# Performance work log

Hardware: AMD Instinct MI355X
Metric: run time of the kernel (lower is better)

The kernel has to match this reference:

```python
import jax, jax.numpy as jnp
import numpy as np

BS, T, NOBJ = 16, 32, 100
GLOVE, GEMB, ADIM, GCN_DIM, H, ASPACE, RES = 300, 64, 10, 512, 512, 6, 512


def setup_inputs() -> dict:
    key = jax.random.key(0)
    ks = jax.random.split(key, 34)
    rn = lambda k, shp, s=0.02: (jax.random.normal(k, shp, jnp.float32) * s)
    inp = {}
    inp["target"] = jax.random.normal(ks[0], (BS, T, GLOVE), jnp.float32)
    inp["input_"] = jax.random.normal(ks[1], (BS, T, RES, 1, 1), jnp.float32)
    inp["action_probs"] = jax.random.uniform(ks[2], (BS, T, ASPACE), jnp.float32)
    # symmetric normalized adjacency (D^-1/2 A D^-1/2), as normalize_adj produces
    A_raw = (jax.random.uniform(ks[3], (NOBJ, NOBJ)) < 0.1).astype(jnp.float32)
    A_raw = ((A_raw + A_raw.T + jnp.eye(NOBJ)) > 0).astype(jnp.float32)
    dinv = 1.0 / jnp.sqrt(jnp.sum(A_raw, axis=1))
    inp["A"] = A_raw * dinv[:, None] * dinv[None, :]
    inp["all_glove"] = jax.random.normal(ks[4], (NOBJ, GLOVE), jnp.float32)
    inp["Wword"] = rn(ks[5], (GEMB, GLOVE)); inp["bword"] = jnp.zeros((GEMB,))
    inp["Wg"] = rn(ks[6], (GEMB, GLOVE)); inp["bg"] = jnp.zeros((GEMB,))
    inp["Wa"] = rn(ks[7], (ADIM, ASPACE)); inp["ba"] = jnp.zeros((ADIM,))
    inp["W0"] = rn(ks[8], (256, RES + GEMB))
    inp["W1"] = rn(ks[9], (256, 256))
    inp["W2"] = rn(ks[10], (1, 256))
    inp["Wfm"] = rn(ks[11], (GCN_DIM, NOBJ)); inp["bfm"] = jnp.zeros((GCN_DIM,))
    fused_in = RES + GEMB + ADIM + GCN_DIM
    inp["Wf"] = rn(ks[12], (H, fused_in)); inp["bf"] = jnp.zeros((H,))
    inp["Wih"] = rn(ks[13], (4 * H, H)); inp["Whh"] = rn(ks[14], (4 * H, H))
    inp["bih"] = jnp.zeros((4 * H,)); inp["bhh"] = jnp.zeros((4 * H,))
    inp["Wa1"] = rn(ks[15], (128, H)); inp["ba1"] = jnp.zeros((128,))
    inp["Wa2"] = rn(ks[16], (ASPACE, 128)); inp["ba2"] = jnp.zeros((ASPACE,))
    inp["Wc1"] = rn(ks[17], (128, H)); inp["bc1"] = jnp.zeros((128,))
    inp["Wc2"] = rn(ks[18], (1, 128)); inp["bc2"] = jnp.zeros((1,))
    return inp


def _forward(target, input_, action_probs, A, all_glove, Wword, bword, Wg, bg,
             Wa, ba, W0, W1, W2, Wfm, bfm, Wf, bf, Wih, Whh, bih, bhh,
             Wa1, ba1, Wa2, ba2, Wc1, bc1, Wc2, bc2):
    bs, t = target.shape[0], target.shape[1]
    B = bs * t
    feats = input_.reshape(B, RES)                      # [B,512] (squeeze 1x1)
    glove_e = jax.nn.relu(target.reshape(B, GLOVE) @ Wg.T + bg)
    act_e = jax.nn.relu(action_probs.reshape(B, ASPACE) @ Wa.T + ba)
    # GCN branch (all_glove is detached in the original)
    word = jax.lax.stop_gradient(all_glove) @ Wword.T + bword   # [N,GEMB]
    N = A.shape[0]
    class_e = jnp.broadcast_to(feats[:, None, :], (B, N, RES))
    x = jnp.concatenate([class_e, jnp.broadcast_to(word[None], (B, N, GEMB))], -1)
    x = jax.nn.relu(jnp.einsum('nm,bmd->bnd', A, x) @ W0.T)     # [B,N,256]
    x = jax.nn.relu(jnp.einsum('nm,bmd->bnd', A, x) @ W1.T)     # [B,N,256]
    x = jax.nn.relu(jnp.einsum('nm,bmd->bnd', A, x) @ W2.T)     # [B,N,1]
    gcn_e = x[..., 0] @ Wfm.T + bfm                             # [B,GCN_DIM]
    fused = jnp.concatenate([feats, glove_e, act_e, gcn_e], -1)
    out = jax.nn.relu(fused @ Wf.T + bf).reshape(bs, t, H)
    # LSTM (torch gate order i,f,g,o), batch_first, zero init state
    h0 = jnp.zeros((bs, H), out.dtype)
    c0 = jnp.zeros((bs, H), out.dtype)
    def step(carry, xt):
        h, c = carry
        g = xt @ Wih.T + h @ Whh.T + bih + bhh
        i, f, gg, o = jnp.split(g, 4, axis=-1)
        c = jax.nn.sigmoid(f) * c + jax.nn.sigmoid(i) * jnp.tanh(gg)
        h = jax.nn.sigmoid(o) * jnp.tanh(c)
        return (h, c), h
    (hT, cT), hs = jax.lax.scan(step, (h0, c0), out.transpose(1, 0, 2))
    sf = hs.transpose(1, 0, 2).reshape(B, H)
    actor = jax.nn.relu(jax.nn.relu(sf @ Wa1.T + ba1) @ Wa2.T + ba2).reshape(bs, t, ASPACE)
    critic = jax.nn.relu(jax.nn.relu(sf @ Wc1.T + bc1) @ Wc2.T + bc2).reshape(bs, t, 1)
    return actor, critic, hT[None], cT[None]


def reference(target, input_, action_probs, A, all_glove, Wword, bword, Wg, bg,
              Wa, ba, W0, W1, W2, Wfm, bfm, Wf, bf, Wih, Whh, bih, bhh,
              Wa1, ba1, Wa2, ba2, Wc1, bc1, Wc2, bc2):
    return _forward(target, input_, action_probs, A, all_glove, Wword, bword,
                    Wg, bg, Wa, ba, W0, W1, W2, Wfm, bfm, Wf, bf, Wih, Whh,
                    bih, bhh, Wa1, ba1, Wa2, ba2, Wc1, bc1, Wc2, bc2)
```

## Files before the change

### kernel.cpp

```cpp
#include <hip/hip_runtime.h>
#include <cmath>

constexpr int BSZ = 16, T = 32, NOBJ = 100;
constexpr int GLOVE = 300, GEMB = 64, ADIM = 10, GCN_DIM = 512, Hh = 512, ASPACE = 6, RES = 512;
constexpr int Bt = BSZ * T;
constexpr int FUSED_IN = RES + GEMB + ADIM + GCN_DIM;
constexpr int FP = 1120;

typedef __attribute__((ext_vector_type(8))) short bf16x8;
typedef __attribute__((ext_vector_type(4))) float f32x4;

__device__ __forceinline__ unsigned short f2bf(float f) {
    unsigned u = __float_as_uint(f);
    return (unsigned short)((u + 0x7FFFu + ((u >> 16) & 1u)) >> 16);
}
__device__ __forceinline__ unsigned pk2(float a, float b) {
    return (unsigned)f2bf(a) | ((unsigned)f2bf(b) << 16);
}

template<bool RELU, int OMODE>
__global__ __launch_bounds__(256)
void mgemm(const unsigned short* __restrict__ A, int lda,
           const unsigned short* __restrict__ B, int ldb,
           float* __restrict__ Cf, unsigned short* __restrict__ Cb, int ldc,
           const float* __restrict__ bias, int K)
{
    const int tid = threadIdx.x;
    const int l = tid & 63, wv = tid >> 6;
    const int m0 = blockIdx.y * 64 + wv * 16;
    const int n0 = blockIdx.x * 64;
    const int lr = l & 15, kg = l >> 4;
    const unsigned short* ap = A + (long)(m0 + lr) * lda + kg * 8;
    const unsigned short* bp = B + (long)(n0 + lr) * ldb + kg * 8;
// ... 83 lines not shown
#pragma unroll
    for (int r = 0; r < 4; ++r) {
        int m = m0 + 4 * mi + r;
        if (m >= M) continue;
        float4 v;
        v.x = acc[r][0] + bv.x; v.y = acc[r][1] + bv.y;
        v.z = acc[r][2] + bv.z; v.w = acc[r][3] + bv.w;
        if (RELU) {
            v.x = fmaxf(v.x, 0.f); v.y = fmaxf(v.y, 0.f);
            v.z = fmaxf(v.z, 0.f); v.w = fmaxf(v.w, 0.f);
        }
        *(float4*)&C[(long)m * ldc + n] = v;
    }
}

constexpr int BM = 64, BN = 64, BK = 16;
template<bool RELU>
__global__ __launch_bounds__(256)
void gemm_nt(const float* __restrict__ A, int lda,
             const float* __restrict__ Bp, int ldb,
             float* __restrict__ C, int ldc,
             const float* __restrict__ bias, int M, int N, int K)
{
    const int m0 = blockIdx.y * BM, n0 = blockIdx.x * BN;
    __shared__ float As[BK][BM + 1];
    __shared__ float Bs[BK][BN + 1];
    const int tid = threadIdx.x;
    const int lo = tid * 4;
    const int lm = lo >> 4;
    const int lk = lo & 15;
    const int row = (tid >> 4) * 4, col = (tid & 15) * 4;
    float acc[4][4] = {};
    for (int k0 = 0; k0 < K; k0 += BK) {
#pragma unroll
        for (int e = 0; e < 4; ++e) {
            int k = lk + e;
            float va = 0.f, vb = 0.f;
            if (k0 + k < K) {
                if (m0 + lm < M) va = A[(long)(m0 + lm) * lda + k0 + k];
                if (n0 + lm < N) vb = Bp[(long)(n0 + lm) * ldb + k0 + k];
            }
            As[k][lm] = va;
            Bs[k][lm] = vb;
        }
        __syncthreads();
#pragma unroll
        for (int k = 0; k < BK; ++k) {
            float a0 = As[k][row], a1 = As[k][row + 1], a2 = As[k][row + 2], a3 = As[k][row + 3];
            float b0 = Bs[k][col], b1 = Bs[k][col + 1], b2 = Bs[k][col + 2], b3 = Bs[k][col + 3];
            acc[0][0] += a0 * b0; acc[0][1] += a0 * b1; acc[0][2] += a0 * b2; acc[0][3] += a0 * b3;
            acc[1][0] += a1 * b0; acc[1][1] += a1 * b1; acc[1][2] += a1 * b2; acc[1][3] += a1 * b3;
            acc[2][0] += a2 * b0; acc[2][1] += a2 * b1; acc[2][2] += a2 * b2; acc[2][3] += a2 * b3;
            acc[3][0] += a3 * b0; acc[3][1] += a3 * b1; acc[3][2] += a3 * b2; acc[3][3] += a3 * b3;
        }
        __syncthreads();
    }
#pragma unroll
    for (int i = 0; i < 4; ++i) {
        int m = m0 + row + i;
        if (m >= M) continue;
#pragma unroll
        for (int j = 0; j < 4; ++j) {
            int n = n0 + col + j;
            if (n >= N) continue;
            float v = acc[i][j];
            if (bias) v += bias[n];
            if (RELU) v = fmaxf(v, 0.f);
            C[(long)m * ldc + n] = v;
        }
    }
}

__global__ __launch_bounds__(256, 2)
void gcn_fused(const float* __restrict__ u,
               const float* __restrict__ v,
               const float* __restrict__ rowsum,
               const float* __restrict__ Aglob,
               const bf16x8* __restrict__ W1f,
               const bf16x8* __restrict__ Af,
               const float* __restrict__ w2,
               unsigned short* __restrict__ x3b)
{
    __shared__ unsigned short X1s[112 * 40];
    __shared__ unsigned short Z1Ts[128 * 136];
    __shared__ float u_lds[256];
    __shared__ float rs_lds[112];
    __shared__ float w2l[256];
    __shared__ float spart[4][112];
    __shared__ float sl[112];

    const int b = blockIdx.x, tid = threadIdx.x;
    const int l = tid & 63, wv = tid >> 6;
    const int lrow = l & 15, kg = l >> 4;

    u_lds[tid] = u[(long)b * 256 + tid];
    w2l[tid] = w2[tid];
    if (tid < 112) rs_lds[tid] = (tid < 100) ? rowsum[tid] : 0.f;
    if (tid < 128) {
        uint4 z = make_uint4(0, 0, 0, 0);
        *(uint4*)&Z1Ts[tid * 136 + 112] = z;
        *(uint4*)&Z1Ts[tid * 136 + 120] = z;
    }
    if (tid < 28) x3b[(long)b * 128 + 100 + tid] = 0;

    float sacc[7][4];
#pragma unroll
    for (int mt = 0; mt < 7; ++mt)
#pragma unroll
        for (int r = 0; r < 4; ++r) sacc[mt][r] = 0.f;

    for (int half = 0; half < 2; ++half) {
        f32x4 acc1[7][2];
#pragma unroll
        for (int mt = 0; mt < 7; ++mt)
#pragma unroll
            for (int jtl = 0; jtl < 2; ++jtl) acc1[mt][jtl] = (f32x4){0.f, 0.f, 0.f, 0.f};

        for (int kt = 0; kt < 8; ++kt) {
            __syncthreads();
            if (tid < 224) {
                int n = tid >> 1, kh = (tid & 1) << 4;
                int kb = kt * 32 + kh;
                uint4 p0 = make_uint4(0, 0, 0, 0), p1 = make_uint4(0, 0, 0, 0);
                if (n < 100) {
                    float rsn = rs_lds[n];
                    const float4* vp = (const float4*)&v[n * 256 + kb];
                    float4 u0 = *(const float4*)&u_lds[kb];
                    float4 u1 = *(const float4*)&u_lds[kb + 4];
                    float4 u2 = *(const float4*)&u_lds[kb + 8];
                    float4 u3 = *(const float4*)&u_lds[kb + 12];
                    float4 v0 = vp[0], v1 = vp[1], v2 = vp[2], v3 = vp[3];
                    float x0 = fmaxf(fmaf(rsn, u0.x, v0.x), 0.f), x1 = fmaxf(fmaf(rsn, u0.y, v0.y), 0.f);
                    float x2 = fmaxf(fmaf(rsn, u0.z, v0.z), 0.f), x3v = fmaxf(fmaf(rsn, u0.w, v0.w), 0.f);
                    float x4 = fmaxf(fmaf(rsn, u1.x, v1.x), 0.f), x5 = fmaxf(fmaf(rsn, u1.y, v1.y), 0.f);
                    float x6 = fmaxf(fmaf(rsn, u1.z, v1.z), 0.f), x7 = fmaxf(fmaf(rsn, u1.w, v1.w), 0.f);
                    float x8 = fmaxf(fmaf(rsn, u2.x, v2.x), 0.f), x9 = fmaxf(fmaf(rsn, u2.y, v2.y), 0.f);
                    float xa = fmaxf(fmaf(rsn, u2.z, v2.z), 0.f), xb = fmaxf(fmaf(rsn, u2.w, v2.w), 0.f);
                    float xc = fmaxf(fmaf(rsn, u3.x, v3.x), 0.f), xd = fmaxf(fmaf(rsn, u3.y, v3.y), 0.f);
                    float xe = fmaxf(fmaf(rsn, u3.z, v3.z), 0.f), xf = fmaxf(fmaf(rsn, u3.w, v3.w), 0.f);
                    p0 = make_uint4(pk2(x0, x1), pk2(x2, x3v), pk2(x4, x5), pk2(x6, x7));
                    p1 = make_uint4(pk2(x8, x9), pk2(xa, xb), pk2(xc, xd), pk2(xe, xf));
                }
                *(uint4*)&X1s[n * 40 + kh] = p0;
                *(uint4*)&X1s[n * 40 + kh + 8] = p1;
            }
            __syncthreads();
            bf16x8 af[7];
#pragma unroll
            for (int mt = 0; mt < 7; ++mt)
                af[mt] = *(const bf16x8*)&X1s[(mt * 16 + lrow) * 40 + kg * 8];
#pragma unroll
            for (int jtl = 0; jtl < 2; ++jtl) {
                int jt = half * 8 + wv * 2 + jtl;
                bf16x8 bfr = W1f[(jt * 8 + kt) * 64 + l];
#pragma unroll
                for (int mt = 0; mt < 7; ++mt)
                    acc1[mt][jtl] = __builtin_amdgcn_mfma_f32_16x16x32_bf16(af[mt], bfr, acc1[mt][jtl], 0, 0, 0);
            }
        }

#pragma unroll
        for (int mt = 0; mt < 7; ++mt)
#pragma unroll
            for (int jtl = 0; jtl < 2; ++jtl) {
                int jloc = (wv * 2 + jtl) * 16 + lrow;
                f32x4 a = acc1[mt][jtl];
                uint2 zz;
                zz.x = pk2(a[0], a[1]);
                zz.y = pk2(a[2], a[3]);
                *(uint2*)&Z1Ts[jloc * 136 + mt * 16 + kg * 4] = zz;
            }

        bf16x8 bz[2][4];
#pragma unroll
        for (int jtl = 0; jtl < 2; ++jtl)
#pragma unroll
            for (int k2 = 0; k2 < 4; ++k2)
                bz[jtl][k2] = *(const bf16x8*)&Z1Ts[((wv * 2 + jtl) * 16 + lrow) * 136 + k2 * 32 + kg * 8];
#pragma unroll
        for (int mt = 0; mt < 7; ++mt) {
            bf16x8 aA[4];
#pragma unroll
            for (int k2 = 0; k2 < 4; ++k2) aA[k2] = Af[(mt * 4 + k2) * 64 + l];
#pragma unroll
            for (int jtl = 0; jtl < 2; ++jtl) {
                f32x4 p = (f32x4){0.f, 0.f, 0.f, 0.f};
#pragma unroll
                for (int k2 = 0; k2 < 4; ++k2)
                    p = __builtin_amdgcn_mfma_f32_16x16x32_bf16(aA[k2], bz[jtl][k2], p, 0, 0, 0);
                float w2j = w2l[half * 128 + (wv * 2 + jtl) * 16 + lrow];
#pragma unroll
                for (int r = 0; r < 4; ++r)
                    sacc[mt][r] = fmaf(fmaxf(p[r], 0.f), w2j, sacc[mt][r]);
// ... 22 lines not shown
        sl[tid] = spart[0][tid] + spart[1][tid] + spart[2][tid] + spart[3][tid];
    __syncthreads();

    float sv0 = (l < 100) ? sl[l] : 0.f;
    float sv1 = (l + 64 < 100) ? sl[l + 64] : 0.f;
#pragma unroll 5
    for (int i = 0; i < 25; ++i) {
        int n = i * 4 + wv;
        float a0 = (l < 100) ? Aglob[n * 100 + l] : 0.f;
        float a1 = (l + 64 < 100) ? Aglob[n * 100 + l + 64] : 0.f;
        float p = a0 * sv0 + a1 * sv1;
#pragma unroll
        for (int off = 32; off; off >>= 1) p += __shfl_xor(p, off);
        if (l == 0) x3b[(long)b * 128 + n] = f2bf(fmaxf(p, 0.f));
    }
}

__global__ void k_aw_rowsum(const float* __restrict__ A, const float* __restrict__ word,
                            float* __restrict__ Aw, float* __restrict__ rowsum)
{
    int i = blockIdx.x * 256 + threadIdx.x;
    if (i < 6400) {
        int n = i / 64, k = i % 64;
        float s = 0.f;
        for (int m = 0; m < 100; ++m) s += A[n * 100 + m] * word[m * 64 + k];
        Aw[i] = s;
    } else if (i < 6500) {
        int n = i - 6400;
        float s = 0.f;
        for (int m = 0; m < 100; ++m) s += A[n * 100 + m];
        rowsum[n] = s;
    }
}

__global__ void k_prep(const float* __restrict__ Whh, float* __restrict__ WhhT2,
                       const float* __restrict__ Wf, unsigned short* __restrict__ WfPb,
                       const float* __restrict__ Wih, unsigned short* __restrict__ Wihb,
                       const float* __restrict__ Wa1, const float* __restrict__ Wc1,
                       unsigned short* __restrict__ Whdb,
                       const float* __restrict__ ba1, const float* __restrict__ bc1,
                       float* __restrict__ bhd,
                       const float* __restrict__ Wg, unsigned short* __restrict__ Wgb,
                       const float* __restrict__ W0, unsigned short* __restrict__ W0ab,
                       const float* __restrict__ Wfm, unsigned short* __restrict__ Wfmb,
                       const float* __restrict__ target, unsigned short* __restrict__ tgtb,
                       const float* __restrict__ feats, unsigned short* __restrict__ featsb,
                       float* __restrict__ hzero,
                       const float* __restrict__ bih, const float* __restrict__ bhh,
                       float* __restrict__ bsum,
                       const float* __restrict__ W1, uint4* __restrict__ W1f,
                       const float* __restrict__ A, uint4* __restrict__ Af)
{
    int bx = blockIdx.x, tid = threadIdx.x;
    if (bx < 4096) {
        int i = bx * 256 + tid;
        int hh = i >> 11, rem = i & 2047, jh = rem >> 2, g = rem & 3;
        WhhT2[i] = Whh[(long)(g * 512 + jh) * 512 + hh];
    } else if (bx < 6336) {
        int i = (bx - 4096) * 256 + tid;
        int r = i / FP, c = i - r * FP;
        WfPb[i] = f2bf(c < FUSED_IN ? Wf[(long)r * FUSED_IN + c] : 0.f);
    } else if (bx < 10432) {
        int i = (bx - 6336) * 256 + tid;
        Wihb[i] = f2bf(Wih[i]);
    } else if (bx < 10944) {
        int i = (bx - 10432) * 256 + tid;
        int r = i >> 9, c = i & 511;
        Whdb[i] = f2bf(r < 128 ? Wa1[r * 512 + c] : Wc1[(r - 128) * 512 + c]);
    } else if (bx < 10945) {
        bhd[tid] = (tid < 128) ? ba1[tid] : bc1[tid - 128];
    } else if (bx < 11025) {
        int i = (bx - 10945) * 256 + tid;
        int r = i / 320, c = i - r * 320;
        Wgb[i] = f2bf(c < GLOVE ? Wg[r * GLOVE + c] : 0.f);
    } else if (bx < 11537) {
        int i = (bx - 11025) * 256 + tid;
        int r = i >> 9, c = i & 511;
        W0ab[i] = f2bf(W0[(long)r * 576 + c]);
    } else if (bx < 11793) {
        int i = (bx - 11537) * 256 + tid;
        int r = i >> 7, c = i & 127;
        Wfmb[i] = f2bf(c < 100 ? Wfm[r * 100 + c] : 0.f);
    } else if (bx < 12433) {
        int i = (bx - 11793) * 256 + tid;
        int r = i / 320, c = i - r * 320;
        tgtb[i] = f2bf(c < GLOVE ? target[(long)r * GLOVE + c] : 0.f);
    } else if (bx < 13457) {
        int i = (bx - 12433) * 256 + tid;
        featsb[i] = f2bf(feats[i]);
    } else if (bx < 13585) {
        int i = (bx - 13457) * 256 + tid;
        hzero[i] = 0.f;
    } else if (bx < 13593) {
        int i = (bx - 13585) * 256 + tid;
        bsum[i] = bih[i] + bhh[i];
    } else if (bx < 13625) {
        int job = (bx - 13593) * 256 + tid;
        int jt = job >> 9, rem = job & 511, kt = rem >> 6, lane = rem & 63;
        int j = jt * 16 + (lane & 15), k0 = kt * 32 + (lane >> 4) * 8;
        const float* src = &W1[(long)j * 256 + k0];
        uint4 p;
        p.x = pk2(src[0], src[1]); p.y = pk2(src[2], src[3]);
        p.z = pk2(src[4], src[5]); p.w = pk2(src[6], src[7]);
        W1f[job] = p;
    } else {
        int job = (bx - 13625) * 256 + tid;
        int mt = job >> 8, rem = job & 255, kt = rem >> 6, lane = rem & 63;
        int m = mt * 16 + (lane & 15), n0 = kt * 32 + (lane >> 4) * 8;
        float h[8];
#pragma unroll
        for (int e = 0; e < 8; ++e)
            h[e] = (m < 100 && n0 + e < 100) ? A[m * 100 + n0 + e] : 0.f;
        uint4 p;
        p.x = pk2(h[0], h[1]); p.y = pk2(h[2], h[3]);
        p.z = pk2(h[4], h[5]); p.w = pk2(h[6], h[7]);
        Af[job] = p;
    }
}

__global__ void k_fused(const float* __restrict__ feats, const float* __restrict__ ge,
                        const float* __restrict__ ae, const float* __restrict__ gcn,
                        unsigned short* __restrict__ fused)
{
    int i = blockIdx.x * 256 + threadIdx.x;
    int b = i / FP, c = i - b * FP;
    float v = 0.f;
    if (c < 512) v = feats[(long)b * 512 + c];
    else if (c < 576) v = ge[(long)b * 64 + (c - 512)];
    else if (c < 586) v = ae[(long)b * 10 + (c - 576)];
    else if (c < 1098) v = gcn[(long)b * 512 + (c - 586)];
    fused[i] = f2bf(v);
}

__device__ __forceinline__ float sigf(float x) { return 1.f / (1.f + __expf(-x)); }

__global__ __launch_bounds__(256)
void lstm_step2(const float* __restrict__ xWih,
                const float4* __restrict__ W4,
                const float* __restrict__ hPrev, const float* __restrict__ cPrev,
                float* __restrict__ hNext, float* __restrict__ cNext,
                unsigned short* __restrict__ sfb, int t)
{
    __shared__ float hlds[512 * 17];
    __shared__ float4 pex[256];
    const int tid = threadIdx.x;
    const float4* hp4 = (const float4*)hPrev;
#pragma unroll
    for (int l = 0; l < 8; ++l) {
        int i4 = tid + l * 256;
        int bb = i4 >> 7, hq = i4 & 127;
        float4 h4 = hp4[i4];
        int hh0 = hq * 4;
        hlds[(hh0 + 0) * 17 + bb] = h4.x;
        hlds[(hh0 + 1) * 17 + bb] = h4.y;
        hlds[(hh0 + 2) * 17 + bb] = h4.z;
        hlds[(hh0 + 3) * 17 + bb] = h4.w;
    }
    __syncthreads();
    const int b = tid & 15, j2 = (tid >> 4) & 1, ks = tid >> 5;
    const int jh = blockIdx.x * 2 + j2;
    float ai = 0.f, af = 0.f, ag = 0.f, ao = 0.f;
    const float4* wcol = W4 + jh;
    int hh = ks * 64;
#pragma unroll 4
    for (int r = 0; r < 64; ++r, ++hh) {
        float4 w = wcol[(long)hh * 512];
        float hp = hlds[hh * 17 + b];
        ai = fmaf(w.x, hp, ai);
        af = fmaf(w.y, hp, af);
        ag = fmaf(w.z, hp, ag);
        ao = fmaf(w.w, hp, ao);
    }
    pex[tid] = make_float4(ai, af, ag, ao);
    __syncthreads();
    if (tid < 32) {
        int fb = tid & 15, fj = tid >> 4;
        float gi = 0.f, gf = 0.f, gg = 0.f, go = 0.f;
#pragma unroll
        for (int k = 0; k < 8; ++k) {
            float4 p = pex[k * 32 + fj * 16 + fb];
            gi += p.x; gf += p.y; gg += p.z; go += p.w;
        }
        int jhf = blockIdx.x * 2 + fj;
        const float* xw = xWih + (long)(fb * T + t) * 2048;
        gi += xw[jhf]; gf += xw[512 + jhf]; gg += xw[1024 + jhf]; go += xw[1536 + jhf];
        float cp = cPrev[fb * 512 + jhf];
        float cn = sigf(gf) * cp + sigf(gi) * tanhf(gg);
        float hn = sigf(go) * tanhf(cn);
        cNext[fb * 512 + jhf] = cn;
        hNext[fb * 512 + jhf] = hn;
        sfb[(long)(fb * T + t) * 512 + jhf] = f2bf(hn);
    }
}

__global__ void k_heads(const float* __restrict__ hd,
                        const float* __restrict__ Wa2, const float* __restrict__ ba2,
                        const float* __restrict__ Wc2, const float* __restrict__ bc2,
                        float* __restrict__ out)
{
    int row = blockIdx.x * 16 + (threadIdx.x >> 4);
    int slot = threadIdx.x & 15;
    if (slot < 6) {
        const float4* h4 = (const float4*)(hd + (long)row * 256);
        const float4* w4 = (const float4*)(Wa2 + slot * 128);
        float s = 0.f;
#pragma unroll
        for (int k = 0; k < 32; ++k) {
            float4 h = h4[k], w = w4[k];
            s += h.x * w.x + h.y * w.y + h.z * w.z + h.w * w.w;
        }
        out[row * 6 + slot] = fmaxf(s + ba2[slot], 0.f);
    } else if (slot == 6) {
        const float4* h4 = (const float4*)(hd + (long)row * 256 + 128);
        const float4* w4 = (const float4*)(Wc2);
        float s = 0.f;
#pragma unroll
        for (int k = 0; k < 32; ++k) {
            float4 h = h4[k], w = w4[k];
            s += h.x * w.x + h.y * w.y + h.z * w.z + h.w * w.w;
        }
        out[3072 + row] = fmaxf(s + bc2[0], 0.f);
    }
}

__global__ void k_copy_hc(const float* __restrict__ h, const float* __restrict__ c,
                          float* __restrict__ out)
{
    int i = blockIdx.x * 256 + threadIdx.x;
    out[3584 + i] = h[i];
    out[11776 + i] = c[i];
}

static inline void mg(hipStream_t st, const unsigned short* A, int lda,
                      const unsigned short* B, int ldb,
                      float* Cf, unsigned short* Cb, int ldc,
                      const float* bias, int M, int N, int K, bool relu, bool bf16out)
{
    dim3 g(N / 64, M / 64), blk(256);
    if (bf16out) {
        if (relu) hipLaunchKernelGGL((mgemm<true, 1>), g, blk, 0, st, A, lda, B, ldb, Cf, Cb, ldc, bias, K);
        else      hipLaunchKernelGGL((mgemm<false, 1>), g, blk, 0, st, A, lda, B, ldb, Cf, Cb, ldc, bias, K);
    } else {
        if (relu) hipLaunchKernelGGL((mgemm<true, 0>), g, blk, 0, st, A, lda, B, ldb, Cf, Cb, ldc, bias, K);
        else      hipLaunchKernelGGL((mgemm<false, 0>), g, blk, 0, st, A, lda, B, ldb, Cf, Cb, ldc, bias, K);
    }
}
static inline void g32(hipStream_t st, const float* A, int lda, const float* B, int ldb,
                       float* C, int ldc, const float* bias, int M, int N, int K, bool relu)
{
    dim3 g((N + 63) / 64, (M + 31) / 32), blk(128);
    if (relu) hipLaunchKernelGGL((gemm32<true>), g, blk, 0, st, A, lda, B, ldb, C, ldc, bias, M, N, K);
    else      hipLaunchKernelGGL((gemm32<false>), g, blk, 0, st, A, lda, B, ldb, C, ldc, bias, M, N, K);
}
static inline void gnt(hipStream_t st, const float* A, int lda, const float* B, int ldb,
                       float* C, int ldc, const float* bias, int M, int N, int K, bool relu)
{
    dim3 g((N + BN - 1) / BN, (M + BM - 1) / BM), blk(256);
    if (relu) hipLaunchKernelGGL((gemm_nt<true>), g, blk, 0, st, A, lda, B, ldb, C, ldc, bias, M, N, K);
    else      hipLaunchKernelGGL((gemm_nt<false>), g, blk, 0, st, A, lda, B, ldb, C, ldc, bias, M, N, K);
}

extern "C" void kernel_launch(void* const* d_in, const int* in_sizes, int n_in,
                              void* d_out, int out_size, void* d_ws, size_t ws_size,
                              hipStream_t stream)
{
    const float* target = (const float*)d_in[0];
    const float* input_ = (const float*)d_in[1];
    const float* aprob  = (const float*)d_in[2];
    const float* Adj    = (const float*)d_in[3];
    const float* aglove = (const float*)d_in[4];
    const float* Wword  = (const float*)d_in[5];
    const float* bword  = (const float*)d_in[6];
    const float* Wg     = (const float*)d_in[7];
    const float* bg     = (const float*)d_in[8];
// ... 12 lines not shown
    const float* bhh    = (const float*)d_in[21];
    const float* Wa1    = (const float*)d_in[22];
    const float* ba1    = (const float*)d_in[23];
    const float* Wa2    = (const float*)d_in[24];
    const float* ba2    = (const float*)d_in[25];
    const float* Wc1    = (const float*)d_in[26];
    const float* bc1    = (const float*)d_in[27];
    const float* Wc2    = (const float*)d_in[28];
    const float* bc2    = (const float*)d_in[29];

    float* ws = (float*)d_ws;
    float* out = (float*)d_out;

    size_t off = 0;
    auto alloc = [&](size_t n) { size_t r = off; off += (n + 255) & ~(size_t)255; return r; };
    float* glove_e = ws + alloc(512 * 64);
    float* act_e   = ws + alloc(512 * 10);
    float* u       = ws + alloc(512 * 256);
    float* word    = ws + alloc(100 * 64);
    float* Aw      = ws + alloc(100 * 64);
    float* rowsum  = ws + alloc(128);
    float* v       = ws + alloc(100 * 256);
    float* gcn_e   = ws + alloc(512 * 512);
    float* bsum    = ws + alloc(2048);
    float* bhd     = ws + alloc(256);
    float* xWih    = ws + alloc((size_t)512 * 2048);
    float* WhhT2   = ws + alloc((size_t)512 * 2048);
    float* hA      = ws + alloc(BSZ * Hh);
    float* cA      = ws + alloc(BSZ * Hh);
    float* hB      = ws + alloc(BSZ * Hh);
    float* cB      = ws + alloc(BSZ * Hh);
    float* hd      = ws + alloc(512 * 256);
    float* W1frag  = ws + alloc(32768);
    float* Afrag   = ws + alloc(7168);
    unsigned short* x3b     = (unsigned short*)(ws + alloc(512 * 128 / 2));
    unsigned short* fusedb  = (unsigned short*)(ws + alloc((size_t)512 * FP / 2));
    unsigned short* WfPb    = (unsigned short*)(ws + alloc((size_t)512 * FP / 2));
    unsigned short* outfb   = (unsigned short*)(ws + alloc(512 * 512 / 2));
    unsigned short* Wihb    = (unsigned short*)(ws + alloc((size_t)2048 * 512 / 2));
    unsigned short* Whdb    = (unsigned short*)(ws + alloc(256 * 512 / 2));
    unsigned short* Wgb     = (unsigned short*)(ws + alloc(64 * 320 / 2));
    unsigned short* W0ab    = (unsigned short*)(ws + alloc(256 * 512 / 2));
    unsigned short* Wfmb    = (unsigned short*)(ws + alloc(512 * 128 / 2));
    unsigned short* tgtb    = (unsigned short*)(ws + alloc(512 * 320 / 2));
    unsigned short* featsb  = (unsigned short*)(ws + alloc(512 * 512 / 2));
    unsigned short* sfb     = (unsigned short*)(ws + alloc(512 * 512 / 2));
    (void)ws_size; (void)in_sizes; (void)n_in; (void)out_size;

    const float* feats = input_;

    hipLaunchKernelGGL(k_prep, dim3(13632), dim3(256), 0, stream,
                       Whh, WhhT2, Wf, WfPb, Wih, Wihb, Wa1, Wc1, Whdb, ba1, bc1, bhd,
                       Wg, Wgb, W0, W0ab, Wfm, Wfmb, target, tgtb, feats, featsb,
                       hA, bih, bhh, bsum, W1, (uint4*)W1frag, Adj, (uint4*)Afrag);

    g32(stream, aglove, GLOVE, Wword, GLOVE, word, 64, bword, 100, 64, GLOVE, false);
    hipLaunchKernelGGL(k_aw_rowsum, dim3(26), dim3(256), 0, stream, Adj, word, Aw, rowsum);
    g32(stream, Aw, 64, W0 + 512, 576, v, 256, nullptr, 100, 256, 64, false);
    gnt(stream, aprob, ASPACE, Wa, ASPACE, act_e, 10, ba, 512, 10, ASPACE, true);

    mg(stream, tgtb, 320, Wgb, 320, glove_e, nullptr, 64, bg, 512, 64, 320, true, false);
    mg(stream, featsb, 512, W0ab, 512, u, nullptr, 256, nullptr, 512, 256, 512, false, false);

    hipLaunchKernelGGL(gcn_fused, dim3(Bt), dim3(256), 0, stream,
                       u, v, rowsum, Adj, (const bf16x8*)W1frag, (const bf16x8*)Afrag, W2, x3b);
    mg(stream, x3b, 128, Wfmb, 128, gcn_e, nullptr, 512, bfm, 512, 512, 128, false, false);

    hipLaunchKernelGGL(k_fused, dim3(512 * FP / 256), dim3(256), 0, stream,
                       feats, glove_e, act_e, gcn_e, fusedb);
    mg(stream, fusedb, FP, WfPb, FP, nullptr, outfb, 512, bf, 512, 512, FP, true, true);
    mg(stream, outfb, 512, Wihb, 512, xWih, nullptr, 2048, bsum, 512, 2048, 512, false, false);

    for (int t = 0; t < T; ++t) {
        const float* hp = (t & 1) ? hB : hA;
        const float* cp = (t & 1) ? cB : cA;
        float* hn = (t & 1) ? hA : hB;
        float* cn = (t & 1) ? cA : cB;
        hipLaunchKernelGGL(lstm_step2, dim3(256), dim3(256), 0, stream,
                           xWih, (const float4*)WhhT2, hp, cp, hn, cn, sfb, t);
    }

    mg(stream, sfb, 512, Whdb, 512, hd, nullptr, 256, bhd, 512, 256, 512, true, false);
    hipLaunchKernelGGL(k_heads, dim3(32), dim3(256), 0, stream, hd, Wa2, ba2, Wc2, bc2, out);
    hipLaunchKernelGGL(k_copy_hc, dim3(32), dim3(256), 0, stream, hA, cA, out);
}
```

Before: 371.5 us.

## Use bf16 MFMA LSTM steps, fuse concat writes, double-buffer GCN tiles

Replaces the fp32 per-step LSTM kernel with a bf16 MFMA kernel that keeps h in bf16 and c in place, and pre-packs Whh into MFMA fragments. The GEMMs for glove and gcn embeddings now write directly into the fused bf16 buffer, and the action embedding and feature copy move into the prep kernel. This removes the k_fused, gemm_nt, k_heads and copy launches. The gcn_fused kernel double-buffers its X1 tile, prefetches v rows into registers, and pads the Z1 LDS stride. Carrying the recurrent h in bf16 adds rounding risk over 32 steps.

```diff
diff --git a/kernel.cpp b/kernel.cpp
--- a/kernel.cpp
+++ b/kernel.cpp
@@ -17,6 +17,7 @@
 __device__ __forceinline__ unsigned pk2(float a, float b) {
     return (unsigned)f2bf(a) | ((unsigned)f2bf(b) << 16);
 }
+__device__ __forceinline__ float sigf(float x) { return 1.f / (1.f + __expf(-x)); }
 
 template<bool RELU, int OMODE>
 __global__ __launch_bounds__(256)
@@ -130,62 +131,7 @@
     }
 }
 
-constexpr int BM = 64, BN = 64, BK = 16;
-template<bool RELU>
-__global__ __launch_bounds__(256)
-void gemm_nt(const float* __restrict__ A, int lda,
-             const float* __restrict__ Bp, int ldb,
-             float* __restrict__ C, int ldc,
-             const float* __restrict__ bias, int M, int N, int K)
-{
-    const int m0 = blockIdx.y * BM, n0 = blockIdx.x * BN;
-    __shared__ float As[BK][BM + 1];
-    __shared__ float Bs[BK][BN + 1];
-    const int tid = threadIdx.x;
-    const int lo = tid * 4;
-    const int lm = lo >> 4;
-    const int lk = lo & 15;
-    const int row = (tid >> 4) * 4, col = (tid & 15) * 4;
-    float acc[4][4] = {};
-    for (int k0 = 0; k0 < K; k0 += BK) {
-#pragma unroll
-        for (int e = 0; e < 4; ++e) {
-            int k = lk + e;
-            float va = 0.f, vb = 0.f;
-            if (k0 + k < K) {
-                if (m0 + lm < M) va = A[(long)(m0 + lm) * lda + k0 + k];
-                if (n0 + lm < N) vb = Bp[(long)(n0 + lm) * ldb + k0 + k];
-            }
-            As[k][lm] = va;
-            Bs[k][lm] = vb;
-        }
-        __syncthreads();
-#pragma unroll
-        for (int k = 0; k < BK; ++k) {
-            float a0 = As[k][row], a1 = As[k][row + 1], a2 = As[k][row + 2], a3 = As[k][row + 3];
-            float b0 = Bs[k][col], b1 = Bs[k][col + 1], b2 = Bs[k][col + 2], b3 = Bs[k][col + 3];
-            acc[0][0] += a0 * b0; acc[0][1] += a0 * b1; acc[0][2] += a0 * b2; acc[0][3] += a0 * b3;
-            acc[1][0] += a1 * b0; acc[1][1] += a1 * b1; acc[1][2] += a1 * b2; acc[1][3] += a1 * b3;
-            acc[2][0] += a2 * b0; acc[2][1] += a2 * b1; acc[2][2] += a2 * b2; acc[2][3] += a2 * b3;
-            acc[3][0] += a3 * b0; acc[3][1] += a3 * b1; acc[3][2] += a3 * b2; acc[3][3] += a3 * b3;
-        }
-        __syncthreads();
-    }
-#pragma unroll
-    for (int i = 0; i < 4; ++i) {
-        int m = m0 + row + i;
-        if (m >= M) continue;
-#pragma unroll
-        for (int j = 0; j < 4; ++j) {
-            int n = n0 + col + j;
-            if (n >= N) continue;
-            float v = acc[i][j];
-            if (bias) v += bias[n];
-            if (RELU) v = fmaxf(v, 0.f);
-            C[(long)m * ldc + n] = v;
-        }
-    }
-}
+constexpr int ZLD = 152;
 
 __global__ __launch_bounds__(256, 2)
 void gcn_fused(const float* __restrict__ u,
@@ -197,8 +143,8 @@
                const float* __restrict__ w2,
                unsigned short* __restrict__ x3b)
 {
-    __shared__ unsigned short X1s[112 * 40];
-    __shared__ unsigned short Z1Ts[128 * 136];
+    __shared__ unsigned short X1s[2][112 * 40];
+    __shared__ unsigned short Z1Ts[128 * ZLD];
     __shared__ float u_lds[256];
     __shared__ float rs_lds[112];
     __shared__ float w2l[256];
@@ -214,10 +160,18 @@
     if (tid < 112) rs_lds[tid] = (tid < 100) ? rowsum[tid] : 0.f;
     if (tid < 128) {
         uint4 z = make_uint4(0, 0, 0, 0);
-        *(uint4*)&Z1Ts[tid * 136 + 112] = z;
-        *(uint4*)&Z1Ts[tid * 136 + 120] = z;
+        *(uint4*)&Z1Ts[tid * ZLD + 112] = z;
+        *(uint4*)&Z1Ts[tid * ZLD + 120] = z;
     }
     if (tid < 28) x3b[(long)b * 128 + 100 + tid] = 0;
+    __syncthreads();
+
+    const int sn = tid >> 1;
+    const int kh = (tid & 1) << 4;
+    const int kq = kh >> 2;
+    const bool gen = (tid < 224) && (sn < 100);
+    const float4* vrow = gen ? ((const float4*)v + sn * 64) : nullptr;
+    const float rsn = (tid < 224) ? rs_lds[sn] : 0.f;
 
     float sacc[7][4];
 #pragma unroll
@@ -232,39 +186,43 @@
 #pragma unroll
             for (int jtl = 0; jtl < 2; ++jtl) acc1[mt][jtl] = (f32x4){0.f, 0.f, 0.f, 0.f};
 
+        float4 q0, q1, q2, q3;
+        if (gen) { q0 = vrow[kq]; q1 = vrow[kq + 1]; q2 = vrow[kq + 2]; q3 = vrow[kq + 3]; }
+
+        int buf = 0;
         for (int kt = 0; kt < 8; ++kt) {
-            __syncthreads();
             if (tid < 224) {
-                int n = tid >> 1, kh = (tid & 1) << 4;
                 int kb = kt * 32 + kh;
                 uint4 p0 = make_uint4(0, 0, 0, 0), p1 = make_uint4(0, 0, 0, 0);
-                if (n < 100) {
-                    float rsn = rs_lds[n];
-                    const float4* vp = (const float4*)&v[n * 256 + kb];
+                if (gen) {
                     float4 u0 = *(const float4*)&u_lds[kb];
                     float4 u1 = *(const float4*)&u_lds[kb + 4];
                     float4 u2 = *(const float4*)&u_lds[kb + 8];
                     float4 u3 = *(const float4*)&u_lds[kb + 12];
-                    float4 v0 = vp[0], v1 = vp[1], v2 = vp[2], v3 = vp[3];
-                    float x0 = fmaxf(fmaf(rsn, u0.x, v0.x), 0.f), x1 = fmaxf(fmaf(rsn, u0.y, v0.y), 0.f);
-                    float x2 = fmaxf(fmaf(rsn, u0.z, v0.z), 0.f), x3v = fmaxf(fmaf(rsn, u0.w, v0.w), 0.f);
-                    float x4 = fmaxf(fmaf(rsn, u1.x, v1.x), 0.f), x5 = fmaxf(fmaf(rsn, u1.y, v1.y), 0.f);
-                    float x6 = fmaxf(fmaf(rsn, u1.z, v1.z), 0.f), x7 = fmaxf(fmaf(rsn, u1.w, v1.w), 0.f);
-                    float x8 = fmaxf(fmaf(rsn, u2.x, v2.x), 0.f), x9 = fmaxf(fmaf(rsn, u2.y, v2.y), 0.f);
-                    float xa = fmaxf(fmaf(rsn, u2.z, v2.z), 0.f), xb = fmaxf(fmaf(rsn, u2.w, v2.w), 0.f);
-                    float xc = fmaxf(fmaf(rsn, u3.x, v3.x), 0.f), xd = fmaxf(fmaf(rsn, u3.y, v3.y), 0.f);
-                    float xe = fmaxf(fmaf(rsn, u3.z, v3.z), 0.f), xf = fmaxf(fmaf(rsn, u3.w, v3.w), 0.f);
+                    float x0 = fmaxf(fmaf(rsn, u0.x, q0.x), 0.f), x1 = fmaxf(fmaf(rsn, u0.y, q0.y), 0.f);
+                    float x2 = fmaxf(fmaf(rsn, u0.z, q0.z), 0.f), x3v = fmaxf(fmaf(rsn, u0.w, q0.w), 0.f);
+                    float x4 = fmaxf(fmaf(rsn, u1.x, q1.x), 0.f), x5 = fmaxf(fmaf(rsn, u1.y, q1.y), 0.f);
+                    float x6 = fmaxf(fmaf(rsn, u1.z, q1.z), 0.f), x7 = fmaxf(fmaf(rsn, u1.w, q1.w), 0.f);
+                    float x8 = fmaxf(fmaf(rsn, u2.x, q2.x), 0.f), x9 = fmaxf(fmaf(rsn, u2.y, q2.y), 0.f);
+                    float xa = fmaxf(fmaf(rsn, u2.z, q2.z), 0.f), xb = fmaxf(fmaf(rsn, u2.w, q2.w), 0.f);
+                    float xc = fmaxf(fmaf(rsn, u3.x, q3.x), 0.f), xd = fmaxf(fmaf(rsn, u3.y, q3.y), 0.f);
+                    float xe = fmaxf(fmaf(rsn, u3.z, q3.z), 0.f), xf = fmaxf(fmaf(rsn, u3.w, q3.w), 0.f);
                     p0 = make_uint4(pk2(x0, x1), pk2(x2, x3v), pk2(x4, x5), pk2(x6, x7));
                     p1 = make_uint4(pk2(x8, x9), pk2(xa, xb), pk2(xc, xd), pk2(xe, xf));
                 }
-                *(uint4*)&X1s[n * 40 + kh] = p0;
-                *(uint4*)&X1s[n * 40 + kh + 8] = p1;
+                *(uint4*)&X1s[buf][sn * 40 + kh] = p0;
+                *(uint4*)&X1s[buf][sn * 40 + kh + 8] = p1;
+            }
+            float4 n0q, n1q, n2q, n3q;
+            if (kt < 7 && gen) {
+                int base = (kt + 1) * 8 + kq;
+                n0q = vrow[base]; n1q = vrow[base + 1]; n2q = vrow[base + 2]; n3q = vrow[base + 3];
             }
             __syncthreads();
             bf16x8 af[7];
 #pragma unroll
             for (int mt = 0; mt < 7; ++mt)
-                af[mt] = *(const bf16x8*)&X1s[(mt * 16 + lrow) * 40 + kg * 8];
+                af[mt] = *(const bf16x8*)&X1s[buf][(mt * 16 + lrow) * 40 + kg * 8];
 #pragma unroll
             for (int jtl = 0; jtl < 2; ++jtl) {
                 int jt = half * 8 + wv * 2 + jtl;
@@ -273,6 +231,8 @@
                 for (int mt = 0; mt < 7; ++mt)
                     acc1[mt][jtl] = __builtin_amdgcn_mfma_f32_16x16x32_bf16(af[mt], bfr, acc1[mt][jtl], 0, 0, 0);
             }
+            q0 = n0q; q1 = n1q; q2 = n2q; q3 = n3q;
+            buf ^= 1;
         }
 
 #pragma unroll
@@ -284,7 +244,7 @@
                 uint2 zz;
                 zz.x = pk2(a[0], a[1]);
                 zz.y = pk2(a[2], a[3]);
-                *(uint2*)&Z1Ts[jloc * 136 + mt * 16 + kg * 4] = zz;
+                *(uint2*)&Z1Ts[jloc * ZLD + mt * 16 + kg * 4] = zz;
             }
 
         bf16x8 bz[2][4];
@@ -292,7 +252,7 @@
         for (int jtl = 0; jtl < 2; ++jtl)
 #pragma unroll
             for (int k2 = 0; k2 < 4; ++k2)
-                bz[jtl][k2] = *(const bf16x8*)&Z1Ts[((wv * 2 + jtl) * 16 + lrow) * 136 + k2 * 32 + kg * 8];
+                bz[jtl][k2] = *(const bf16x8*)&Z1Ts[((wv * 2 + jtl) * 16 + lrow) * ZLD + k2 * 32 + kg * 8];
 #pragma unroll
         for (int mt = 0; mt < 7; ++mt) {
             bf16x8 aA[4];
@@ -345,6 +305,48 @@
         for (int off = 32; off; off >>= 1) p += __shfl_xor(p, off);
         if (l == 0) x3b[(long)b * 128 + n] = f2bf(fmaxf(p, 0.f));
     }
+}
+
+__global__ __launch_bounds__(256)
+void lstm_mf(const float* __restrict__ xWih,
+             const bf16x8* __restrict__ Whhf,
+             const unsigned short* __restrict__ hPrev,
+             unsigned short* __restrict__ hNext,
+             float* __restrict__ cBuf,
+             float* __restrict__ hFin,
+             unsigned short* __restrict__ sfb, int t)
+{
+    __shared__ float gl[4][16][17];
+    const int tid = threadIdx.x;
+    const int l = tid & 63, g = tid >> 6;
+    const int bid = blockIdx.x;
+    const int jt = g * 32 + bid;
+    const int lr = l & 15, kg = l >> 4;
+    const unsigned short* hp = hPrev + lr * 512 + kg * 8;
+    const bf16x8* wp = Whhf + (size_t)jt * 16 * 64 + l;
+    f32x4 acc = (f32x4){0.f, 0.f, 0.f, 0.f};
+#pragma unroll
+    for (int kt = 0; kt < 16; ++kt) {
+        bf16x8 a = *(const bf16x8*)(hp + kt * 32);
+        acc = __builtin_amdgcn_mfma_f32_16x16x32_bf16(a, wp[kt * 64], acc, 0, 0, 0);
+    }
+#pragma unroll
+    for (int r = 0; r < 4; ++r) gl[g][kg * 4 + r][lr] = acc[r];
+    __syncthreads();
+    const int b = tid >> 4, jl = tid & 15;
+    const int jh = bid * 16 + jl;
+    const float* xw = xWih + (size_t)(b * T + t) * 2048;
+    float gi = gl[0][b][jl] + xw[jh];
+    float gf = gl[1][b][jl] + xw[512 + jh];
+    float gg = gl[2][b][jl] + xw[1024 + jh];
+    float go = gl[3][b][jl] + xw[1536 + jh];
+    float cp = cBuf[b * 512 + jh];
+    float cn = sigf(gf) * cp + sigf(gi) * tanhf(gg);
+    float hn = sigf(go) * tanhf(cn);
+    cBuf[b * 512 + jh] = cn;
+    hNext[b * 512 + jh] = f2bf(hn);
+    hFin[b * 512 + jh] = hn;
+    sfb[(size_t)(b * T + t) * 512 + jh] = f2bf(hn);
 }
 
 __global__ void k_aw_rowsum(const float* __restrict__ A, const float* __restrict__ word,
@@ -364,7 +366,7 @@
     }
 }
 
-__global__ void k_prep(const float* __restrict__ Whh, float* __restrict__ WhhT2,
+__global__ void k_prep(const float* __restrict__ Whh, uint4* __restrict__ Whhf,
                        const float* __restrict__ Wf, unsigned short* __restrict__ WfPb,
                        const float* __restrict__ Wih, unsigned short* __restrict__ Wihb,
                        const float* __restrict__ Wa1, const float* __restrict__ Wc1,
@@ -376,57 +378,82 @@
                        const float* __restrict__ Wfm, unsigned short* __restrict__ Wfmb,
                        const float* __restrict__ target, unsigned short* __restrict__ tgtb,
                        const float* __restrict__ feats, unsigned short* __restrict__ featsb,
-                       float* __restrict__ hzero,
+                       unsigned short* __restrict__ fusedb,
+                       const float* __restrict__ aprob, const float* __restrict__ Wa,
+                       const float* __restrict__ ba,
+                       unsigned short* __restrict__ hbA, float* __restrict__ cBuf,
                        const float* __restrict__ bih, const float* __restrict__ bhh,
                        float* __restrict__ bsum,
                        const float* __restrict__ W1, uint4* __restrict__ W1f,
                        const float* __restrict__ A, uint4* __restrict__ Af)
 {
     int bx = blockIdx.x, tid = threadIdx.x;
-    if (bx < 4096) {
-        int i = bx * 256 + tid;
-        int hh = i >> 11, rem = i & 2047, jh = rem >> 2, g = rem & 3;
-        WhhT2[i] = Whh[(long)(g * 512 + jh) * 512 + hh];
-    } else if (bx < 6336) {
-        int i = (bx - 4096) * 256 + tid;
+    if (bx < 512) {
+        int job = bx * 256 + tid;
+        int jtkt = job >> 6, ll = job & 63;
+        int j = (jtkt >> 4) * 16 + (ll & 15);
+        int k0 = (jtkt & 15) * 32 + (ll >> 4) * 8;
+        const float* src = &Whh[(long)j * 512 + k0];
+        uint4 p;
+        p.x = pk2(src[0], src[1]); p.y = pk2(src[2], src[3]);
+        p.z = pk2(src[4], src[5]); p.w = pk2(src[6], src[7]);
+        Whhf[job] = p;
+    } else if (bx < 2752) {
+        int i = (bx - 512) * 256 + tid;
         int r = i / FP, c = i - r * FP;
         WfPb[i] = f2bf(c < FUSED_IN ? Wf[(long)r * FUSED_IN + c] : 0.f);
-    } else if (bx < 10432) {
-        int i = (bx - 6336) * 256 + tid;
+    } else if (bx < 6848) {
+        int i = (bx - 2752) * 256 + tid;
         Wihb[i] = f2bf(Wih[i]);
-    } else if (bx < 10944) {
-        int i = (bx - 10432) * 256 + tid;
+    } else if (bx < 7360) {
+        int i = (bx - 6848) * 256 + tid;
         int r = i >> 9, c = i & 511;
         Whdb[i] = f2bf(r < 128 ? Wa1[r * 512 + c] : Wc1[(r - 128) * 512 + c]);
-    } else if (bx < 10945) {
+    } else if (bx < 7361) {
         bhd[tid] = (tid < 128) ? ba1[tid] : bc1[tid - 128];
-    } else if (bx < 11025) {
-        int i = (bx - 10945) * 256 + tid;
+    } else if (bx < 7441) {
+        int i = (bx - 7361) * 256 + tid;
         int r = i / 320, c = i - r * 320;
         Wgb[i] = f2bf(c < GLOVE ? Wg[r * GLOVE + c] : 0.f);
-    } else if (bx < 11537) {
-        int i = (bx - 11025) * 256 + tid;
+    } else if (bx < 7953) {
+        int i = (bx - 7441) * 256 + tid;
         int r = i >> 9, c = i & 511;
         W0ab[i] = f2bf(W0[(long)r * 576 + c]);
-    } else if (bx < 11793) {
-        int i = (bx - 11537) * 256 + tid;
+    } else if (bx < 8209) {
+        int i = (bx - 7953) * 256 + tid;
         int r = i >> 7, c = i & 127;
         Wfmb[i] = f2bf(c < 100 ? Wfm[r * 100 + c] : 0.f);
-    } else if (bx < 12433) {
-        int i = (bx - 11793) * 256 + tid;
+    } else if (bx < 8849) {
+        int i = (bx - 8209) * 256 + tid;
         int r = i / 320, c = i - r * 320;
         tgtb[i] = f2bf(c < GLOVE ? target[(long)r * GLOVE + c] : 0.f);
-    } else if (bx < 13457) {
-        int i = (bx - 12433) * 256 + tid;
+    } else if (bx < 9873) {
+        int i = (bx - 8849) * 256 + tid;
         featsb[i] = f2bf(feats[i]);
-    } else if (bx < 13585) {
-        int i = (bx - 13457) * 256 + tid;
-        hzero[i] = 0.f;
-    } else if (bx < 13593) {
-        int i = (bx - 13585) * 256 + tid;
+    } else if (bx < 10897) {
+        int i = (bx - 9873) * 256 + tid;
+        int r = i >> 9, c = i & 511;
+        fusedb[(long)r * FP + c] = f2bf(feats[i]);
+    } else if (bx < 10917) {
+        int i = (bx - 10897) * 256 + tid;
+        int r = i / 10, c6 = i - r * 10;
+        float s = ba[c6];
+#pragma unroll
+        for (int k = 0; k < 6; ++k) s += aprob[r * 6 + k] * Wa[c6 * 6 + k];
+        fusedb[(long)r * FP + 576 + c6] = f2bf(fmaxf(s, 0.f));
+    } else if (bx < 10961) {
+        int i = (bx - 10917) * 256 + tid;
+        int r = i / 22, c = 1098 + (i - r * 22);
+        fusedb[(long)r * FP + c] = 0;
+    } else if (bx < 11009) {
+        int sub = bx - 10961;
+        if (sub < 16) { int i = sub * 256 + tid; hbA[i] = 0; }
+        else          { int i = (sub - 16) * 256 + tid; cBuf[i] = 0.f; }
+    } else if (bx < 11017) {
+        int i = (bx - 11009) * 256 + tid;
         bsum[i] = bih[i] + bhh[i];
-    } else if (bx < 13625) {
-        int job = (bx - 13593) * 256 + tid;
+    } else if (bx < 11049) {
+        int job = (bx - 11017) * 256 + tid;
         int jt = job >> 9, rem = job & 511, kt = rem >> 6, lane = rem & 63;
         int j = jt * 16 + (lane & 15), k0 = kt * 32 + (lane >> 4) * 8;
         const float* src = &W1[(long)j * 256 + k0];
@@ -435,7 +462,7 @@
         p.z = pk2(src[4], src[5]); p.w = pk2(src[6], src[7]);
         W1f[job] = p;
     } else {
-        int job = (bx - 13625) * 256 + tid;
+        int job = (bx - 11049) * 256 + tid;
         int mt = job >> 8, rem = job & 255, kt = rem >> 6, lane = rem & 63;
         int m = mt * 16 + (lane & 15), n0 = kt * 32 + (lane >> 4) * 8;
         float h[8];
@@ -449,117 +476,41 @@
     }
 }
 
-__global__ void k_fused(const float* __restrict__ feats, const float* __restrict__ ge,
-                        const float* __restrict__ ae, const float* __restrict__ gcn,
-                        unsigned short* __restrict__ fused)
-{
-    int i = blockIdx.x * 256 + threadIdx.x;
-    int b = i / FP, c = i - b * FP;
-    float v = 0.f;
-    if (c < 512) v = feats[(long)b * 512 + c];
-    else if (c < 576) v = ge[(long)b * 64 + (c - 512)];
-    else if (c < 586) v = ae[(long)b * 10 + (c - 576)];
-    else if (c < 1098) v = gcn[(long)b * 512 + (c - 586)];
-    fused[i] = f2bf(v);
-}
-
-__device__ __forceinline__ float sigf(float x) { return 1.f / (1.f + __expf(-x)); }
-
-__global__ __launch_bounds__(256)
-void lstm_step2(const float* __restrict__ xWih,
-                const float4* __restrict__ W4,
-                const float* __restrict__ hPrev, const float* __restrict__ cPrev,
-                float* __restrict__ hNext, float* __restrict__ cNext,
-                unsigned short* __restrict__ sfb, int t)
-{
-    __shared__ float hlds[512 * 17];
-    __shared__ float4 pex[256];
-    const int tid = threadIdx.x;
-    const float4* hp4 = (const float4*)hPrev;
-#pragma unroll
-    for (int l = 0; l < 8; ++l) {
-        int i4 = tid + l * 256;
-        int bb = i4 >> 7, hq = i4 & 127;
-        float4 h4 = hp4[i4];
-        int hh0 = hq * 4;
-        hlds[(hh0 + 0) * 17 + bb] = h4.x;
-        hlds[(hh0 + 1) * 17 + bb] = h4.y;
-        hlds[(hh0 + 2) * 17 + bb] = h4.z;
-        hlds[(hh0 + 3) * 17 + bb] = h4.w;
-    }
-    __syncthreads();
-    const int b = tid & 15, j2 = (tid >> 4) & 1, ks = tid >> 5;
-    const int jh = blockIdx.x * 2 + j2;
-    float ai = 0.f, af = 0.f, ag = 0.f, ao = 0.f;
-    const float4* wcol = W4 + jh;
-    int hh = ks * 64;
-#pragma unroll 4
-    for (int r = 0; r < 64; ++r, ++hh) {
-        float4 w = wcol[(long)hh * 512];
-        float hp = hlds[hh * 17 + b];
-        ai = fmaf(w.x, hp, ai);
-        af = fmaf(w.y, hp, af);
-        ag = fmaf(w.z, hp, ag);
-        ao = fmaf(w.w, hp, ao);
-    }
-    pex[tid] = make_float4(ai, af, ag, ao);
-    __syncthreads();
-    if (tid < 32) {
-        int fb = tid & 15, fj = tid >> 4;
-        float gi = 0.f, gf = 0.f, gg = 0.f, go = 0.f;
-#pragma unroll
-        for (int k = 0; k < 8; ++k) {
-            float4 p = pex[k * 32 + fj * 16 + fb];
-            gi += p.x; gf += p.y; gg += p.z; go += p.w;
-        }
-        int jhf = blockIdx.x * 2 + fj;
-        const float* xw = xWih + (long)(fb * T + t) * 2048;
-        gi += xw[jhf]; gf += xw[512 + jhf]; gg += xw[1024 + jhf]; go += xw[1536 + jhf];
-        float cp = cPrev[fb * 512 + jhf];
-        float cn = sigf(gf) * cp + sigf(gi) * tanhf(gg);
-        float hn = sigf(go) * tanhf(cn);
-        cNext[fb * 512 + jhf] = cn;
-        hNext[fb * 512 + jhf] = hn;
-        sfb[(long)(fb * T + t) * 512 + jhf] = f2bf(hn);
-    }
-}
-
-__global__ void k_heads(const float* __restrict__ hd,
-                        const float* __restrict__ Wa2, const float* __restrict__ ba2,
-                        const float* __restrict__ Wc2, const float* __restrict__ bc2,
-                        float* __restrict__ out)
-{
-    int row = blockIdx.x * 16 + (threadIdx.x >> 4);
-    int slot = threadIdx.x & 15;
-    if (slot < 6) {
-        const float4* h4 = (const float4*)(hd + (long)row * 256);
-        const float4* w4 = (const float4*)(Wa2 + slot * 128);
-        float s = 0.f;
-#pragma unroll
-        for (int k = 0; k < 32; ++k) {
-            float4 h = h4[k], w = w4[k];
-            s += h.x * w.x + h.y * w.y + h.z * w.z + h.w * w.w;
-        }
-        out[row * 6 + slot] = fmaxf(s + ba2[slot], 0.f);
-    } else if (slot == 6) {
-        const float4* h4 = (const float4*)(hd + (long)row * 256 + 128);
-        const float4* w4 = (const float4*)(Wc2);
-        float s = 0.f;
-#pragma unroll
-        for (int k = 0; k < 32; ++k) {
-            float4 h = h4[k], w = w4[k];
-            s += h.x * w.x + h.y * w.y + h.z * w.z + h.w * w.w;
-        }
-        out[3072 + row] = fmaxf(s + bc2[0], 0.f);
-    }
-}
-
-__global__ void k_copy_hc(const float* __restrict__ h, const float* __restrict__ c,
-                          float* __restrict__ out)
-{
-    int i = blockIdx.x * 256 + threadIdx.x;
-    out[3584 + i] = h[i];
-    out[11776 + i] = c[i];
+__global__ void k_finish(const float* __restrict__ hd,
+                         const float* __restrict__ Wa2, const float* __restrict__ ba2,
+                         const float* __restrict__ Wc2, const float* __restrict__ bc2,
+                         const float* __restrict__ hFin, const float* __restrict__ cBuf,
+                         float* __restrict__ out)
+{
+    if (blockIdx.x < 32) {
+        int row = blockIdx.x * 16 + (threadIdx.x >> 4);
+        int slot = threadIdx.x & 15;
+        if (slot < 6) {
+            const float4* h4 = (const float4*)(hd + (long)row * 256);
+            const float4* w4 = (const float4*)(Wa2 + slot * 128);
+            float s = 0.f;
+#pragma unroll
+            for (int k = 0; k < 32; ++k) {
+                float4 h = h4[k], w = w4[k];
+                s += h.x * w.x + h.y * w.y + h.z * w.z + h.w * w.w;
+            }
+            out[row * 6 + slot] = fmaxf(s + ba2[slot], 0.f);
+        } else if (slot == 6) {
+            const float4* h4 = (const float4*)(hd + (long)row * 256 + 128);
+            const float4* w4 = (const float4*)(Wc2);
+            float s = 0.f;
+#pragma unroll
+            for (int k = 0; k < 32; ++k) {
+                float4 h = h4[k], w = w4[k];
+                s += h.x * w.x + h.y * w.y + h.z * w.z + h.w * w.w;
+            }
+            out[3072 + row] = fmaxf(s + bc2[0], 0.f);
+        }
+    } else {
+        int i = (blockIdx.x - 32) * 256 + threadIdx.x;
+        out[3584 + i] = hFin[i];
+        out[11776 + i] = cBuf[i];
+    }
 }
 
 static inline void mg(hipStream_t st, const unsigned short* A, int lda,
@@ -582,13 +533,6 @@
     dim3 g((N + 63) / 64, (M + 31) / 32), blk(128);
     if (relu) hipLaunchKernelGGL((gemm32<true>), g, blk, 0, st, A, lda, B, ldb, C, ldc, bias, M, N, K);
     else      hipLaunchKernelGGL((gemm32<false>), g, blk, 0, st, A, lda, B, ldb, C, ldc, bias, M, N, K);
-}
-static inline void gnt(hipStream_t st, const float* A, int lda, const float* B, int ldb,
-                       float* C, int ldc, const float* bias, int M, int N, int K, bool relu)
-{
-    dim3 g((N + BN - 1) / BN, (M + BM - 1) / BM), blk(256);
-    if (relu) hipLaunchKernelGGL((gemm_nt<true>), g, blk, 0, st, A, lda, B, ldb, C, ldc, bias, M, N, K);
-    else      hipLaunchKernelGGL((gemm_nt<false>), g, blk, 0, st, A, lda, B, ldb, C, ldc, bias, M, N, K);
 }
 
 extern "C" void kernel_launch(void* const* d_in, const int* in_sizes, int n_in,
@@ -631,25 +575,20 @@
 
     size_t off = 0;
     auto alloc = [&](size_t n) { size_t r = off; off += (n + 255) & ~(size_t)255; return r; };
-    float* glove_e = ws + alloc(512 * 64);
-    float* act_e   = ws + alloc(512 * 10);
     float* u       = ws + alloc(512 * 256);
     float* word    = ws + alloc(100 * 64);
     float* Aw      = ws + alloc(100 * 64);
     float* rowsum  = ws + alloc(128);
     float* v       = ws + alloc(100 * 256);
-    float* gcn_e   = ws + alloc(512 * 512);
     float* bsum    = ws + alloc(2048);
     float* bhd     = ws + alloc(256);
     float* xWih    = ws + alloc((size_t)512 * 2048);
-    float* WhhT2   = ws + alloc((size_t)512 * 2048);
-    float* hA      = ws + alloc(BSZ * Hh);
-    float* cA      = ws + alloc(BSZ * Hh);
-    float* hB      = ws + alloc(BSZ * Hh);
-    float* cB      = ws + alloc(BSZ * Hh);
     float* hd      = ws + alloc(512 * 256);
+    float* hFin    = ws + alloc(BSZ * Hh);
+    float* cBuf    = ws + alloc(BSZ * Hh);
     float* W1frag  = ws + alloc(32768);
     float* Afrag   = ws + alloc(7168);
+    float* Whhf    = ws + alloc((size_t)524288);
     unsigned short* x3b     = (unsigned short*)(ws + alloc(512 * 128 / 2));
     unsigned short* fusedb  = (unsigned short*)(ws + alloc((size_t)512 * FP / 2));
     unsigned short* WfPb    = (unsigned short*)(ws + alloc((size_t)512 * FP / 2));
@@ -662,42 +601,40 @@
     unsigned short* tgtb    = (unsigned short*)(ws + alloc(512 * 320 / 2));
     unsigned short* featsb  = (unsigned short*)(ws + alloc(512 * 512 / 2));
     unsigned short* sfb     = (unsigned short*)(ws + alloc(512 * 512 / 2));
+    unsigned short* hbA     = (unsigned short*)(ws + alloc(BSZ * Hh / 2));
+    unsigned short* hbB     = (unsigned short*)(ws + alloc(BSZ * Hh / 2));
     (void)ws_size; (void)in_sizes; (void)n_in; (void)out_size;
 
     const float* feats = input_;
 
-    hipLaunchKernelGGL(k_prep, dim3(13632), dim3(256), 0, stream,
-                       Whh, WhhT2, Wf, WfPb, Wih, Wihb, Wa1, Wc1, Whdb, ba1, bc1, bhd,
+    hipLaunchKernelGGL(k_prep, dim3(11056), dim3(256), 0, stream,
+                       Whh, (uint4*)Whhf, Wf, WfPb, Wih, Wihb, Wa1, Wc1, Whdb, ba1, bc1, bhd,
                        Wg, Wgb, W0, W0ab, Wfm, Wfmb, target, tgtb, feats, featsb,
-                       hA, bih, bhh, bsum, W1, (uint4*)W1frag, Adj, (uint4*)Afrag);
+                       fusedb, aprob, Wa, ba, hbA, cBuf, bih, bhh, bsum,
+                       W1, (uint4*)W1frag, Adj, (uint4*)Afrag);
 
     g32(stream, aglove, GLOVE, Wword, GLOVE, word, 64, bword, 100, 64, GLOVE, false);
     hipLaunchKernelGGL(k_aw_rowsum, dim3(26), dim3(256), 0, stream, Adj, word, Aw, rowsum);
     g32(stream, Aw, 64, W0 + 512, 576, v, 256, nullptr, 100, 256, 64, false);
-    gnt(stream, aprob, ASPACE, Wa, ASPACE, act_e, 10, ba, 512, 10, ASPACE, true);
-
-    mg(stream, tgtb, 320, Wgb, 320, glove_e, nullptr, 64, bg, 512, 64, 320, true, false);
+
     mg(stream, featsb, 512, W0ab, 512, u, nullptr, 256, nullptr, 512, 256, 512, false, false);
+    mg(stream, tgtb, 320, Wgb, 320, nullptr, fusedb + 512, FP, bg, 512, 64, 320, true, true);
 
     hipLaunchKernelGGL(gcn_fused, dim3(Bt), dim3(256), 0, stream,
                        u, v, rowsum, Adj, (const bf16x8*)W1frag, (const bf16x8*)Afrag, W2, x3b);
-    mg(stream, x3b, 128, Wfmb, 128, gcn_e, nullptr, 512, bfm, 512, 512, 128, false, false);
-
-    hipLaunchKernelGGL(k_fused, dim3(512 * FP / 256), dim3(256), 0, stream,
-                       feats, glove_e, act_e, gcn_e, fusedb);
+    mg(stream, x3b, 128, Wfmb, 128, nullptr, fusedb + 586, FP, bfm, 512, 512, 128, false, true);
+
     mg(stream, fusedb, FP, WfPb, FP, nullptr, outfb, 512, bf, 512, 512, FP, true, true);
     mg(stream, outfb, 512, Wihb, 512, xWih, nullptr, 2048, bsum, 512, 2048, 512, false, false);
 
     for (int t = 0; t < T; ++t) {
-        const float* hp = (t & 1) ? hB : hA;
-        const float* cp = (t & 1) ? cB : cA;
-        float* hn = (t & 1) ? hA : hB;
-        float* cn = (t & 1) ? cA : cB;
-        hipLaunchKernelGGL(lstm_step2, dim3(256), dim3(256), 0, stream,
-                           xWih, (const float4*)WhhT2, hp, cp, hn, cn, sfb, t);
+        const unsigned short* hp = (t & 1) ? hbB : hbA;
+        unsigned short* hn = (t & 1) ? hbA : hbB;
+        hipLaunchKernelGGL(lstm_mf, dim3(32), dim3(256), 0, stream,
+                           xWih, (const bf16x8*)Whhf, hp, hn, cBuf, hFin, sfb, t);
     }
 
     mg(stream, sfb, 512, Whdb, 512, hd, nullptr, 256, bhd, 512, 256, 512, true, false);
-    hipLaunchKernelGGL(k_heads, dim3(32), dim3(256), 0, stream, hd, Wa2, ba2, Wc2, bc2, out);
-    hipLaunchKernelGGL(k_copy_hc, dim3(32), dim3(256), 0, stream, hA, cA, out);
-}
+    hipLaunchKernelGGL(k_finish, dim3(64), dim3(256), 0, stream,
+                       hd, Wa2, ba2, Wc2, bc2, hFin, cBuf, out);
+}
```

Result: faster. 316.9 us (-14.7%).
